# Kernel optimization log

Measured on AMD Instinct MI355X. Metric: run time of the kernel, lower is better.

The kernel has to match this reference:

```python
import jax, jax.numpy as jnp
import numpy as np

N, C, K, KEIG, B, NG, H = 32768, 128, 5, 128, 64, 512, 4
E = 524288
EPS = 1e-5


def setup_inputs() -> dict:
    key = jax.random.key(0)
    ks = iter(jax.random.split(key, 40))
    def nrm(shape, scale):
        return jax.random.normal(next(ks), shape, jnp.float32) * scale
    s = 1.0 / np.sqrt(C)
    return dict(
        x=nrm((N, C), 1.0),
        U=nrm((N, KEIG), 1.0 / np.sqrt(N)),
        Lambda=jax.random.uniform(next(ks), (KEIG,), jnp.float32, 0.0, 2.0),
        lambda_max=jnp.full((1,), 2.0, jnp.float32),
        w_spa1=nrm((C, C), s), b_spa1=jnp.zeros((C,), jnp.float32),
        w_spa2=nrm((C, C), s), b_spa2=jnp.zeros((C,), jnp.float32),
        w_spe1=nrm((C, C), s), b_spe1=jnp.zeros((C,), jnp.float32),
        w_spe2=nrm((C, C), s), b_spe2=jnp.zeros((C,), jnp.float32),
        cheb_w=nrm((K, C, C), s), cheb_b=jnp.zeros((C,), jnp.float32),
        gamma=jnp.ones((1,), jnp.float32),
        w_proj=nrm((C, C), s),
        w_qkv=nrm((C, 3 * C), s), b_qkv=jnp.zeros((3 * C,), jnp.float32),
        w_out=nrm((C, C), s), b_out=jnp.zeros((C,), jnp.float32),
        mlp_w1=nrm((C, 2 * C), s), mlp_b1=jnp.zeros((2 * C,), jnp.float32),
        mlp_w2=nrm((2 * C, C), 1.0 / np.sqrt(2 * C)), mlp_b2=jnp.zeros((C,), jnp.float32),
        bn1_w=jnp.ones((C,), jnp.float32), bn1_b=jnp.zeros((C,), jnp.float32),
        bn2_w=jnp.ones((C,), jnp.float32), bn2_b=jnp.zeros((C,), jnp.float32),
        bn3_w=jnp.ones((C,), jnp.float32), bn3_b=jnp.zeros((C,), jnp.float32),
        edge_index=jax.random.randint(next(ks), (2, E), 0, N, jnp.int64) if jax.config.jax_enable_x64 else jax.random.randint(next(ks), (2, E), 0, N, jnp.int32),
        batch=jnp.repeat(jnp.arange(B), NG),  # 64 graphs of 512 nodes each
    )


def _mlp2(h, w1, b1, w2, b2):
    return jnp.maximum(h @ w1 + b1, 0.0) @ w2 + b2


def _bn(h, w, b):
    # train-mode BatchNorm1d over node dim (biased variance), GPSConv default norm
    mu = h.mean(0)
    var = jnp.mean((h - mu) ** 2, 0)
    return (h - mu) * jax.lax.rsqrt(var + EPS) * w + b


def _cheb(x, src, dst, lam, Ws, bias):
    # L_hat = (2/lambda_max) * (I - D^{-1/2} A D^{-1/2}) - I ; sym normalization
    deg = jax.ops.segment_sum(jnp.ones_like(src, x.dtype), src, num_segments=N)
    dis = jnp.where(deg > 0, 1.0 / jnp.sqrt(deg), 0.0)
    w = dis[src] * dis[dst]  # [E]
    scale = 2.0 / lam
    def lhat(v):
        agg = jax.ops.segment_sum(w[:, None] * v[src], dst, num_segments=N)
        return (scale - 1.0) * v - scale * agg
    Tx0 = x
    out = Tx0 @ Ws[0]
    Tx1 = lhat(Tx0)
    out = out + Tx1 @ Ws[1]
    for k in range(2, K):
        Tx2 = 2.0 * lhat(Tx1) - Tx0
        out = out + Tx2 @ Ws[k]
        Tx0, Tx1 = Tx1, Tx2
    return out + bias


def _mha(xd, w_qkv, b_qkv, w_out, b_out):
    Bq, n, _ = xd.shape
    dh = C // H
    qkv = xd @ w_qkv + b_qkv  # [B,n,3C]
    q, k, v = jnp.split(qkv, 3, axis=-1)
    heads = lambda t: t.reshape(Bq, n, H, dh).transpose(0, 2, 1, 3)
    q, k, v = heads(q), heads(k), heads(v)
    a = jax.nn.softmax(jnp.einsum('bhqd,bhkd->bhqk', q, k) / np.sqrt(dh), axis=-1)
    o = jnp.einsum('bhqk,bhkd->bhqd', a, v).transpose(0, 2, 1, 3).reshape(Bq, n, C)
    return o @ w_out + b_out


def reference(x, U, Lambda, lambda_max,
              w_spa1, b_spa1, w_spa2, b_spa2,
              w_spe1, b_spe1, w_spe2, b_spe2,
              cheb_w, cheb_b, gamma, w_proj,
              w_qkv, b_qkv, w_out, b_out,
              mlp_w1, mlp_b1, mlp_w2, mlp_b2,
              bn1_w, bn1_b, bn2_w, bn2_b, bn3_w, bn3_b,
              edge_index, batch):
    src, dst = edge_index[0], edge_index[1]
    lam = lambda_max[0]
    # ---- SpectralLocalNN (GPSConv local conv branch) ----
    x_sp = _mlp2(x, w_spa1, b_spa1, w_spa2, b_spa2)
    out_local = _cheb(x_sp, src, dst, lam, cheb_w, cheb_b)
    x_spec = _mlp2(x, w_spe1, b_spe1, w_spe2, b_spe2)
    h_proj = x_spec @ w_proj
    s_lam = jnp.exp(-gamma[0] * Lambda ** 2)  # [k_eig]
    out_spectral = U @ (s_lam[:, None] * (U.T @ h_proj))
    h1 = _bn(out_local + out_spectral + x, bn1_w, bn1_b)
    # ---- global attention branch (equal-size graphs -> dense reshape) ----
    xd = x.reshape(B, NG, C)
    h2 = _mha(xd, w_qkv, b_qkv, w_out, b_out).reshape(N, C)
    h2 = _bn(h2 + x, bn2_w, bn2_b)
    # ---- combine + MLP ----
    out = h1 + h2
    out = out + _mlp2(out, mlp_w1, mlp_b1, mlp_w2, mlp_b2)
    return _bn(out, bn3_w, bn3_b)
```

## Files before the change

### kernel.cpp

```cpp
#include <hip/hip_runtime.h>

typedef short bf16x8 __attribute__((ext_vector_type(8)));
typedef short bf16x4 __attribute__((ext_vector_type(4)));
typedef float f32x4 __attribute__((ext_vector_type(4)));

#define DEVI __device__ __forceinline__

constexpr int N   = 32768;
constexpr int C   = 128;
constexpr int E   = 524288;
constexpr float EPSV = 1e-5f;
constexpr int UT_BLOCKS = 256;
constexpr int HB  = 64;
constexpr int EPB = E / HB;
constexpr float QSCALE = 0.17677669529663687f * 1.4426950408889634f;

DEVI float bf2f(ushort u){ return __uint_as_float(((uint)u) << 16); }
DEVI ushort f2bf(float f){
  uint u = __float_as_uint(f);
  return (ushort)((u + 0x7fffu + ((u >> 16) & 1u)) >> 16);
}
DEVI uint cvtpk(float lo, float hi){
  uint r;
  asm("v_cvt_pk_bf16_f32 %0, %1, %2" : "=v"(r) : "v"(lo), "v"(hi));
  return r;
}
DEVI float fexp2(float x){
  float r;
  asm("v_exp_f32 %0, %1" : "=v"(r) : "v"(x));
  return r;
}
DEVI float sane(float v){ if (!(v == v)) return 0.f; return fminf(fmaxf(v, -1e30f), 1e30f); }
DEVI bool mode_fp32(const uint* lmraw){ return (lmraw[0] & 0xffffu) == 0u; }

constexpr int CSZ[28] = {128,1,16384,128,16384,128,16384,128,16384,128,81920,128,
                         1,16384,49152,384,16384,128,32768,256,32768,128,
                         128,128,128,128,128,128};
constexpr int COF[28] = {0,128,192,16576,16704,33088,33216,49600,49728,66112,
                         66240,148160,148288,148352,164736,213888,214272,230656,
                         230784,263552,263808,296576,296704,296832,296960,297088,
                         297216,297344};
constexpr int CAN_SMALL_TOTAL = 297472;

struct CvtArgs { const void* src[28]; };

__global__ __launch_bounds__(256) void convert_small(CvtArgs a, ushort* __restrict__ can,
                                                     const uint* __restrict__ lmraw)
{
  bool f32 = mode_fp32(lmraw);
  int idx = blockIdx.x * 256 + threadIdx.x;
  #pragma unroll 1
  for (int s = 0; s < 28; s++) {
    if (idx < CSZ[s]) {
      ushort v = f32 ? f2bf(((const float*)a.src[s])[idx])
                     : ((const ushort*)a.src[s])[idx];
      can[COF[s] + idx] = v;
      return;
    }
    idx -= CSZ[s];
  }
}

__global__ __launch_bounds__(256) void convert_big(const void* __restrict__ xs,
    const void* __restrict__ Us, ushort* __restrict__ canx, ushort* __restrict__ canu,
    const uint* __restrict__ lmraw)
{
  bool f32 = mode_fp32(lmraw);
  size_t e = ((size_t)blockIdx.x * 256 + threadIdx.x) * 4;
  bool isU = e >= (size_t)N * C;
  size_t off = isU ? e - (size_t)N * C : e;
  const void* src = isU ? Us : xs;
  ushort* dst = isU ? canu : canx;
  ushort4 o;
  if (f32) {
    float4 v = *(const float4*)((const float*)src + off);
    o.x = f2bf(v.x); o.y = f2bf(v.y); o.z = f2bf(v.z); o.w = f2bf(v.w);
  } else {
    o = *(const ushort4*)((const ushort*)src + off);
  }
  *(ushort4*)(dst + off) = o;
}

__global__ __launch_bounds__(1024) void hist_lds(const int* __restrict__ ei,
    int* __restrict__ cei, ushort* __restrict__ part)
{
  __shared__ uint hist[N / 2];
  int t = threadIdx.x;
  int b = blockIdx.x;
  bool i64 = ((ei[1] | ei[3] | ei[5] | ei[7]) == 0);
  size_t j0 = (size_t)b * EPB;
  #pragma unroll
  for (int i = t; i < N / 2; i += 1024) hist[i] = 0u;
  __syncthreads();
  for (int k = t; k < EPB; k += 1024) {
    size_t j = j0 + k;
    int v = (i64 ? ei[2 * j] : ei[j]) & (N - 1);
    cei[j] = v;
    atomicAdd(&hist[v >> 1], 1u << ((v & 1) * 16));
  }
  __syncthreads();
  uint* po = (uint*)(part + (size_t)b * N);
  for (int i = t; i < N / 2; i += 1024) po[i] = hist[i];
}

__global__ __launch_bounds__(256) void reduce_cnt(const ushort* __restrict__ part,
    int* __restrict__ cdt, float* __restrict__ dis)
{
  int d = blockIdx.x * 256 + threadIdx.x;
  int s = 0, tt = 0;
  #pragma unroll 8
  for (int b = 0; b < HB; b++) s  += part[(size_t)b * N + d];
  #pragma unroll 8
  for (int b = 0; b < HB; b++) tt += part[(size_t)(HB + b) * N + d];
  cdt[d] = tt;
  dis[d] = s > 0 ? rsqrtf((float)s) : 0.f;
}

__global__ __launch_bounds__(1024) void scan_kernel(const int* __restrict__ cnt,
                                                    int* __restrict__ row_ptr)
{
  __shared__ int sums[1024];
  int t = threadIdx.x;
  int loc[32]; int s = 0;
  int base = t * 32;
  #pragma unroll
  for (int i = 0; i < 32; i++) { loc[i] = s; s += cnt[base + i]; }
  sums[t] = s;
  __syncthreads();
  for (int off = 1; off < 1024; off <<= 1) {
    int v = (t >= off) ? sums[t - off] : 0;
    __syncthreads();
    sums[t] += v;
    __syncthreads();
  }
  int pre = (t == 0) ? 0 : sums[t - 1];
  #pragma unroll
  for (int i = 0; i < 32; i++) row_ptr[base + i] = pre + loc[i];
}

__global__ __launch_bounds__(256) void off_kernel(const int* __restrict__ rp,
    const ushort* __restrict__ part, int* __restrict__ off2)
{
  int d = blockIdx.x * 256 + threadIdx.x;
  int run = rp[d];
  #pragma unroll 8
  for (int b = 0; b < HB; b++) {
    off2[(size_t)b * N + d] = run;
    run += part[(size_t)(HB + b) * N + d];
  }
}

__global__ __launch_bounds__(1024) void edge_scatter(const int* __restrict__ cei,
    const int* __restrict__ off2, const float* __restrict__ dis,
    int2* __restrict__ ep)
{
  __shared__ int base[N];
  int t = threadIdx.x;
  int b = blockIdx.x;
  for (int i = t; i < N; i += 1024) base[i] = off2[(size_t)b * N + i];
  __syncthreads();
  size_t e0 = (size_t)b * EPB;
  for (int k = t; k < EPB; k += 1024) {
    size_t e = e0 + k;
    int s = cei[e], d = cei[e + E];
    int slot = atomicAdd(&base[d], 1);
    int2 v; v.x = s; v.y = __float_as_int(dis[s] * dis[d]);
    ep[slot] = v;
  }
}

constexpr int WT_SPA1 = 0;
constexpr int WT_SPA2 = 16384;
constexpr int WT_SPE1 = 32768;
constexpr int WT_SPE2 = 49152;
constexpr int WT_PROJ = 65536;
constexpr int WT_CHEB = 81920;
constexpr int WT_QKV  = 163840;
constexpr int WT_WOUT = 212992;
constexpr int WT_MLP1 = 229376;
constexpr int WT_MLP2 = 262144;
constexpr int WT_TOTAL = 294912;

__global__ __launch_bounds__(256) void zero_kernel(int* __restrict__ p, int n)
{
  int i = blockIdx.x * 256 + threadIdx.x;
  if (i < n) p[i] = 0;
}

__global__ __launch_bounds__(256) void transpose_weights(
    const ushort* __restrict__ spa1, const ushort* __restrict__ spa2,
    const ushort* __restrict__ spe1, const ushort* __restrict__ spe2,
    const ushort* __restrict__ proj, const ushort* __restrict__ cheb,
    const ushort* __restrict__ qkv,  const ushort* __restrict__ wout,
    const ushort* __restrict__ mlp1, const ushort* __restrict__ mlp2,
    ushort* __restrict__ wt)
{
  int i = blockIdx.x * 256 + threadIdx.x;
  if (i < 81920) {
    int m = i >> 14, r = i & 16383; int k = r >> 7, n = r & 127;
    const ushort* src = m==0?spa1 : m==1?spa2 : m==2?spe1 : m==3?spe2 : proj;
    wt[m*16384 + n*128 + k] = src[r];
  } else if (i < 163840) {
    int j = i - 81920; int m = j >> 14, r = j & 16383; int k = r >> 7, n = r & 127;
    wt[WT_CHEB + n*640 + m*128 + k] = cheb[j];
  } else if (i < 212992) {
    int j = i - 163840; int k = j / 384, n = j % 384;
    wt[WT_QKV + n*128 + k] = qkv[j];
  } else if (i < 229376) {
    int j = i - 212992; int k = j >> 7, n = j & 127;
    wt[WT_WOUT + n*128 + k] = wout[j];
  } else if (i < 262144) {
    int j = i - 229376; int k = j >> 8, n = j & 255;
    wt[WT_MLP1 + n*128 + k] = mlp1[j];
  } else if (i < WT_TOTAL) {
    int j = i - 262144; int k = j >> 7, n = j & 127;
    wt[WT_MLP2 + n*256 + k] = mlp2[j];
  }
}

template<int K, int COLS, bool RELU, int OMODE, bool BIAS, bool RES, int ASTR, int OSTR, bool QSC>
__global__ __launch_bounds__(256) void gemm_lds(
    const ushort* __restrict__ A, const ushort* __restrict__ WT,
    const ushort* __restrict__ bias, const ushort* __restrict__ res,
    void* __restrict__ outp)
{
  constexpr int NSEG = COLS / 128;
  constexpr int NKC = K / 128;
  constexpr int BP = 136;
  __shared__ ushort Bs[128 * BP];
  int tid = threadIdx.x;
  int lane = tid & 63, wave = tid >> 6;
  int quad = lane >> 4, l16 = lane & 15;
  int seg = (NSEG > 1) ? (blockIdx.x % NSEG) : 0;
  int rb  = (NSEG > 1) ? (blockIdx.x / NSEG) : blockIdx.x;
  int row0 = rb * 64 + wave * 16;
  const ushort* wseg = WT + (size_t)(seg * 128) * K;

  f32x4 acc[8];
  #pragma unroll
  for (int nt = 0; nt < 8; nt++) acc[nt] = (f32x4){0.f, 0.f, 0.f, 0.f};

  for (int kc = 0; kc < NKC; kc++) {
    if (kc) __syncthreads();
    #pragma unroll
    for (int i = tid; i < 2048; i += 256) {
      int col = i >> 4, ko = (i & 15) * 8;
      *(bf16x8*)&Bs[col * BP + ko] =
          *(const bf16x8*)(wseg + (size_t)col * K + kc * 128 + ko);
    }
    __syncthreads();
    bf16x8 a[4];
    const ushort* ap = A + (size_t)(row0 + l16) * ASTR + kc * 128 + quad * 8;
    #pragma unroll
    for (int kk = 0; kk < 4; kk++) a[kk] = *(const bf16x8*)(ap + kk * 32);
    #pragma unroll
    for (int kk = 0; kk < 4; kk++) {
      #pragma unroll
      for (int nt = 0; nt < 8; nt++) {
        bf16x8 b = *(const bf16x8*)(&Bs[(nt * 16 + l16) * BP + kk * 32 + quad * 8]);
        acc[nt] = __builtin_amdgcn_mfma_f32_16x16x32_bf16(a[kk], b, acc[nt], 0, 0, 0);
      }
    }
  }

  #pragma unroll
  for (int nt = 0; nt < 8; nt++) {
    int col = seg * 128 + nt * 16 + l16;
    float bv = 0.f;
    if (BIAS) bv = bf2f(bias[col]);
    #pragma unroll
    for (int r = 0; r < 4; r++) {
      int row = row0 + quad * 4 + r;
      size_t oi = (size_t)row * OSTR + col;
      float v = acc[nt][r] + bv;
      if (RES) v += bf2f(res[(size_t)row * COLS + col]);
      if (RELU) v = fmaxf(v, 0.f);
      if (QSC && col < 128) v *= QSCALE;
      if (OMODE == 0)      ((ushort*)outp)[oi] = f2bf(v);
      else if (OMODE == 1) ((float*)outp)[oi] = v;
      else                 ((float*)outp)[oi] += v;
    }
  }
}

__global__ __launch_bounds__(256) void spmm_cheb(
    const int* __restrict__ row_ptr, const int2* __restrict__ ep,
    const ushort* __restrict__ v,
    const ushort* __restrict__ txprev, ushort* __restrict__ txout,
    const ushort* __restrict__ lambda_max, int first, int str)
{
  int wave = threadIdx.x >> 6, lane = threadIdx.x & 63;
  int sub = lane >> 4, l16 = lane & 15;
  int d = blockIdx.x * 4 + wave;
  float lm = bf2f(lambda_max[0]);
  float scale = 2.f / lm;
  if (!(scale == scale) || fabsf(scale) > 1e6f) scale = 1.f;
  int beg = row_ptr[d];
  int end = (d == N - 1) ? E : row_ptr[d + 1];
  float acc[8] = {0.f,0.f,0.f,0.f,0.f,0.f,0.f,0.f};
  for (int jb = beg; jb < end; jb += 4) {
    int j = jb + sub;
    bool ok = j < end;
    int2 e2 = ep[ok ? j : beg];
    int s = e2.x & (N - 1);
    float w = ok ? __int_as_float(e2.y) : 0.f;
    bf16x8 vv = *(const bf16x8*)(v + (size_t)s * str + l16 * 8);
    #pragma unroll
    for (int i = 0; i < 8; i++) acc[i] += w * bf2f((ushort)vv[i]);
  }
  #pragma unroll
  for (int i = 0; i < 8; i++) {
    acc[i] += __shfl_xor(acc[i], 16);
    acc[i] += __shfl_xor(acc[i], 32);
  }
  if (sub == 0) {
    bf16x8 vd = *(const bf16x8*)(v + (size_t)d * str + l16 * 8);
    bf16x8 tp;
    if (!first) tp = *(const bf16x8*)(txprev + (size_t)d * str + l16 * 8);
    bf16x8 ov;
    #pragma unroll
    for (int i = 0; i < 8; i++) {
      float r = (scale - 1.f) * bf2f((ushort)vd[i]) - scale * acc[i];
      if (!first) r = 2.f * r - bf2f((ushort)tp[i]);
      ov[i] = (short)f2bf(r);
    }
    *(bf16x8*)(txout + (size_t)d * str + l16 * 8) = ov;
  }
}

__global__ __launch_bounds__(256) void ut_mfma(const ushort* __restrict__ U,
    const ushort* __restrict__ hp, float* __restrict__ parts)
{
  constexpr int RP = 40;
  __shared__ ushort Ut[128 * RP];
  __shared__ ushort Ht[128 * RP];
  int t = threadIdx.x;
  int lane = t & 63, wave = t >> 6;
  int quad = lane >> 4, l16 = lane & 15;

  f32x4 acc[2][8];
  #pragma unroll
  for (int a = 0; a < 2; a++)
    #pragma unroll
    for (int ct = 0; ct < 8; ct++) acc[a][ct] = (f32x4){0.f, 0.f, 0.f, 0.f};

  for (int ch = 0; ch < 4; ch++) {
    int n0 = blockIdx.x * 128 + ch * 32;
    __syncthreads();
    for (int i = t; i < 2048; i += 256) {
      int r2 = i >> 7, c = i & 127;
      uint u0 = U [(size_t)(n0 + r2 * 2) * 128 + c];
      uint u1 = U [(size_t)(n0 + r2 * 2 + 1) * 128 + c];
      *(uint*)&Ut[c * RP + r2 * 2] = (u0 & 0xffffu) | (u1 << 16);
      uint h0 = hp[(size_t)(n0 + r2 * 2) * 128 + c];
      uint h1 = hp[(size_t)(n0 + r2 * 2 + 1) * 128 + c];
      *(uint*)&Ht[c * RP + r2 * 2] = (h0 & 0xffffu) | (h1 << 16);
    }
    __syncthreads();
    bf16x8 bfr[8];
    #pragma unroll
    for (int ct = 0; ct < 8; ct++)
      bfr[ct] = *(const bf16x8*)(&Ht[(ct * 16 + l16) * RP + quad * 8]);
    #pragma unroll
    for (int a = 0; a < 2; a++) {
      int kt = wave * 2 + a;
      bf16x8 af = *(const bf16x8*)(&Ut[(kt * 16 + l16) * RP + quad * 8]);
      #pragma unroll
      for (int ct = 0; ct < 8; ct++)
        acc[a][ct] = __builtin_amdgcn_mfma_f32_16x16x32_bf16(af, bfr[ct], acc[a][ct], 0, 0, 0);
    }
  }

  float* po = parts + (size_t)blockIdx.x * 16384;
  #pragma unroll
  for (int a = 0; a < 2; a++) {
    int kt = wave * 2 + a;
    #pragma unroll
    for (int ct = 0; ct < 8; ct++)
      #pragma unroll
      for (int r = 0; r < 4; r++)
        po[(kt * 16 + quad * 4 + r) * 128 + ct * 16 + l16] = acc[a][ct][r];
  }
}

__global__ __launch_bounds__(256) void reduce_mt(const float* __restrict__ parts,
    const ushort* __restrict__ Lambda, const ushort* __restrict__ gamma,
    ushort* __restrict__ MT)
{
  int e = blockIdx.x * 256 + threadIdx.x;
  int keig = e >> 7, c = e & 127;
  float s = 0.f;
  for (int p = 0; p < UT_BLOCKS; p++) s += parts[(size_t)p * 16384 + e];
  float g = bf2f(gamma[0]);
  float lam = bf2f(Lambda[keig]);
  float sl = __expf(-g * lam * lam);
  MT[c * 128 + keig] = f2bf(sl * s);
}

__global__ __launch_bounds__(256) void bn_stats(const float* __restrict__ h,
                                                float* __restrict__ stats)
{
  int c = threadIdx.x & 127, half = threadIdx.x >> 7;
  int r0 = blockIdx.x * 128 + half;
  float s = 0.f, s2 = 0.f;
  for (int i = 0; i < 64; i++) {
    float v = sane(h[(size_t)(r0 + i * 2) * 128 + c]);
    s += v; s2 += v * v;
  }
  atomicAdd(&stats[c], s);
  atomicAdd(&stats[128 + c], s2);
}

__global__ __launch_bounds__(256) void bn_apply(const float* __restrict__ h,
    const float* __restrict__ st, const ushort* __restrict__ gw,
    const ushort* __restrict__ gb, const ushort* __restrict__ add,
    void* __restrict__ out, const uint* __restrict__ lmraw, int final_out)
{
  size_t e = ((size_t)blockIdx.x * 256 + threadIdx.x) * 4;
  int c0 = (int)(e & 127);
  float4 hv = *(const float4*)(h + e);
  float xv[4] = {sane(hv.x), sane(hv.y), sane(hv.z), sane(hv.w)};
  float addv[4] = {0.f, 0.f, 0.f, 0.f};
  if (add) {
    ushort4 av = *(const ushort4*)(add + e);
    addv[0] = bf2f(av.x); addv[1] = bf2f(av.y);
    addv[2] = bf2f(av.z); addv[3] = bf2f(av.w);
  }
  float r[4];
  #pragma unroll
  for (int j = 0; j < 4; j++) {
    int c = c0 + j;
    float mu = st[c] * (1.f / 32768.f);
    float var = fmaxf(st[128 + c] * (1.f / 32768.f) - mu * mu, 0.f);
    r[j] = (xv[j] - mu) * rsqrtf(var + EPSV) * bf2f(gw[c]) + bf2f(gb[c]) + addv[j];
  }
  if (final_out && mode_fp32(lmraw)) {
    float4 o4; o4.x = r[0]; o4.y = r[1]; o4.z = r[2]; o4.w = r[3];
    *(float4*)((float*)out + e) = o4;
  } else {
    ushort4 o;
    o.x = f2bf(r[0]); o.y = f2bf(r[1]); o.z = f2bf(r[2]); o.w = f2bf(r[3]);
    *(ushort4*)((ushort*)out + e) = o;
  }
}

__global__ __launch_bounds__(512) void attn_mfma(const ushort* __restrict__ qkv,
                                                 ushort* __restrict__ attn)
{
  constexpr int VP = 516;
  constexpr int KP = 40;
  __shared__ ushort Kt[512 * KP];
  __shared__ ushort Vt[32 * VP];
  int b = blockIdx.x;
  int g = b >> 3, hh = (b >> 1) & 3, half = b & 1;
  int lane = threadIdx.x & 63, wave = threadIdx.x >> 6;
  int quad = lane >> 4, l16 = lane & 15;
  const ushort* base = qkv + (size_t)g * 512 * 384;

  for (int i = threadIdx.x; i < 512 * 4; i += 512) {
    int key = i >> 2, c8 = (i & 3) * 8;
    *(bf16x8*)&Kt[key * KP + c8] =
        *(const bf16x8*)(base + (size_t)key * 384 + 128 + hh * 32 + c8);
  }
  for (int i = threadIdx.x; i < 256 * 8; i += 512) {
    int kp = i >> 3, d4 = (i & 7) * 4;
    const ushort* va = base + (size_t)(2 * kp) * 384 + 256 + hh * 32 + d4;
    ushort4 a = *(const ushort4*)va;
    ushort4 c = *(const ushort4*)(va + 384);
    *(uint*)&Vt[(d4 + 0) * VP + 2 * kp] = (uint)a.x | ((uint)c.x << 16);
    *(uint*)&Vt[(d4 + 1) * VP + 2 * kp] = (uint)a.y | ((uint)c.y << 16);
    *(uint*)&Vt[(d4 + 2) * VP + 2 * kp] = (uint)a.z | ((uint)c.z << 16);
    *(uint*)&Vt[(d4 + 3) * VP + 2 * kp] = (uint)a.w | ((uint)c.w << 16);
  }
  __syncthreads();

  int q0 = half * 256 + wave * 32;
  bf16x8 qf[2];
  #pragma unroll
  for (int i = 0; i < 2; i++)
    qf[i] = *(const bf16x8*)(base + (size_t)(q0 + i * 16 + l16) * 384 + hh * 32 + quad * 8);

  f32x4 O[2][2];
  #pragma unroll
  for (int dt = 0; dt < 2; dt++)
    #pragma unroll
    for (int i = 0; i < 2; i++) O[dt][i] = (f32x4){0.f, 0.f, 0.f, 0.f};
  float lsum[2] = {0.f, 0.f};

  union PU { uint u[4]; bf16x8 v; };
  union VU { uint2 a[2]; bf16x8 v; };

  for (int kt2 = 0; kt2 < 16; kt2++) {
    int k0 = kt2 * 32;
    bf16x8 kfA = *(const bf16x8*)&Kt[(k0 + l16) * KP + quad * 8];
    bf16x8 kfB = *(const bf16x8*)&Kt[(k0 + 16 + l16) * KP + quad * 8];
    PU pw[2];
    #pragma unroll
    for (int i = 0; i < 2; i++) {
      f32x4 sA = __builtin_amdgcn_mfma_f32_16x16x32_bf16(kfA, qf[i], (f32x4){0.f,0.f,0.f,0.f}, 0, 0, 0);
      f32x4 sB = __builtin_amdgcn_mfma_f32_16x16x32_bf16(kfB, qf[i], (f32x4){0.f,0.f,0.f,0.f}, 0, 0, 0);
      float p0 = fexp2(fminf(sA[0], 86.5f));
      float p1 = fexp2(fminf(sA[1], 86.5f));
      float p2 = fexp2(fminf(sA[2], 86.5f));
      float p3 = fexp2(fminf(sA[3], 86.5f));
      float p4 = fexp2(fminf(sB[0], 86.5f));
      float p5 = fexp2(fminf(sB[1], 86.5f));
      float p6 = fexp2(fminf(sB[2], 86.5f));
      float p7 = fexp2(fminf(sB[3], 86.5f));
      lsum[i] += ((p0 + p1) + (p2 + p3)) + ((p4 + p5) + (p6 + p7));
      pw[i].u[0] = cvtpk(p0, p1); pw[i].u[1] = cvtpk(p2, p3);
      pw[i].u[2] = cvtpk(p4, p5); pw[i].u[3] = cvtpk(p6, p7);
    }
    #pragma unroll
    for (int dt = 0; dt < 2; dt++) {
      int drow = (dt * 16 + l16) * VP;
      VU vu;
      vu.a[0] = *(const uint2*)&Vt[drow + k0 + quad * 4];
      vu.a[1] = *(const uint2*)&Vt[drow + k0 + 16 + quad * 4];
      #pragma unroll
      for (int i = 0; i < 2; i++)
        O[dt][i] = __builtin_amdgcn_mfma_f32_16x16x32_bf16(vu.v, pw[i].v, O[dt][i], 0, 0, 0);
    }
  }

  #pragma unroll
  for (int i = 0; i < 2; i++) {
    float l = lsum[i];
    l += __shfl_xor(l, 16);
    l += __shfl_xor(l, 32);
    lsum[i] = 1.f / l;
  }

  #pragma unroll
  for (int i = 0; i < 2; i++) {
    size_t node = (size_t)g * 512 + q0 + i * 16 + l16;
    #pragma unroll
    for (int dt = 0; dt < 2; dt++) {
      uint2 o;
      o.x = cvtpk(O[dt][i][0] * lsum[i], O[dt][i][1] * lsum[i]);
      o.y = cvtpk(O[dt][i][2] * lsum[i], O[dt][i][3] * lsum[i]);
      *(uint2*)(attn + node * 128 + hh * 32 + dt * 16 + quad * 4) = o;
    }
  }
}

constexpr size_t KB = 1024;
constexpr size_t MB = 1048576;
constexpr size_t OFF_WT    = 0;
constexpr size_t OFF_CDT   = 576 * KB;
constexpr size_t OFF_RP    = 704 * KB;
constexpr size_t OFF_DIS   = 832 * KB;
constexpr size_t OFF_MT    = 960 * KB;
constexpr size_t OFF_STATS = 1024 * KB;
constexpr size_t OFF_CEI   = 6  * MB;
constexpr size_t OFF_EP    = 10 * MB;
constexpr size_t OFF_CANX  = 14 * MB;
constexpr size_t OFF_CANU  = 22 * MB;
constexpr size_t OFF_CANS  = 30 * MB;
constexpr size_t OFF_F1    = 31 * MB;
constexpr size_t OFF_SPEC  = 31 * MB;
constexpr size_t OFF_HPROJ = 39 * MB;
constexpr size_t OFF_TBIG  = 47 * MB;
constexpr size_t OFF_PARTH = OFF_TBIG;
constexpr size_t OFF_OFF2  = OFF_TBIG + 8 * MB;
constexpr size_t OFF_PARTS = 87 * MB;

extern "C" void kernel_launch(void* const* d_in, const int* in_sizes, int n_in,
                              void* d_out, int out_size, void* d_ws, size_t ws_size,
                              hipStream_t stream) {
  (void)in_sizes; (void)n_in; (void)out_size; (void)ws_size;
  const uint* lmraw = (const uint*)d_in[3];
  const int*  ei    = (const int*)d_in[30];

  char* W = (char*)d_ws;
  ushort* wt    = (ushort*)(W + OFF_WT);
  int*    cdt   = (int*)(W + OFF_CDT);
  int*    rp    = (int*)(W + OFF_RP);
  float*  dis   = (float*)(W + OFF_DIS);
  ushort* MT    = (ushort*)(W + OFF_MT);
  float*  stats = (float*)(W + OFF_STATS);
  int*    cei   = (int*)(W + OFF_CEI);
  int2*   ep    = (int2*)(W + OFF_EP);
  ushort* part  = (ushort*)(W + OFF_PARTH);
  int*    off2  = (int*)(W + OFF_OFF2);
  ushort* canx  = (ushort*)(W + OFF_CANX);
  ushort* canu  = (ushort*)(W + OFF_CANU);
  ushort* cs    = (ushort*)(W + OFF_CANS);
  float*  F1    = (float*)(W + OFF_F1);
  ushort* spec  = (ushort*)(W + OFF_SPEC);
  ushort* tmpA  = (ushort*)(W + OFF_HPROJ);
  ushort* hproj = (ushort*)(W + OFF_HPROJ);
  ushort* Tbig  = (ushort*)(W + OFF_TBIG);
  ushort* qkvb  = (ushort*)(W + OFF_TBIG);
  ushort* mlph  = (ushort*)(W + OFF_TBIG);
  float*  parts = (float*)(W + OFF_PARTS);
  ushort* attnb = (ushort*)(W + OFF_PARTS);
  ushort* h1    = (ushort*)(W + OFF_CANU);
  ushort* comb  = (ushort*)(W + OFF_CANX);

  const ushort* cLambda = cs + COF[0];
  const ushort* cLmx    = cs + COF[1];
  const ushort* cSpa1   = cs + COF[2];
  const ushort* cBspa1  = cs + COF[3];
  const ushort* cSpa2   = cs + COF[4];
  const ushort* cBspa2  = cs + COF[5];
  const ushort* cSpe1   = cs + COF[6];
  const ushort* cBspe1  = cs + COF[7];
  const ushort* cSpe2   = cs + COF[8];
  const ushort* cBspe2  = cs + COF[9];
  const ushort* cCheb   = cs + COF[10];
  const ushort* cChebB  = cs + COF[11];
  const ushort* cGam    = cs + COF[12];
  const ushort* cProj   = cs + COF[13];
  const ushort* cQkv    = cs + COF[14];
  const ushort* cBqkv   = cs + COF[15];
  const ushort* cWout   = cs + COF[16];
  const ushort* cBout   = cs + COF[17];
  const ushort* cMw1    = cs + COF[18];
  const ushort* cMb1    = cs + COF[19];
  const ushort* cMw2    = cs + COF[20];
  const ushort* cMb2    = cs + COF[21];
  const ushort* cBn1w   = cs + COF[22];
  const ushort* cBn1b   = cs + COF[23];
  const ushort* cBn2w   = cs + COF[24];
  const ushort* cBn2b   = cs + COF[25];
  const ushort* cBn3w   = cs + COF[26];
  const ushort* cBn3b   = cs + COF[27];

  const ushort* NUL = nullptr;

  zero_kernel<<<3, 256, 0, stream>>>((int*)(W + OFF_STATS), 768);

  CvtArgs ca;
  ca.src[0]  = d_in[2];  ca.src[1]  = d_in[3];  ca.src[2]  = d_in[4];
  ca.src[3]  = d_in[5];  ca.src[4]  = d_in[6];  ca.src[5]  = d_in[7];
  ca.src[6]  = d_in[8];  ca.src[7]  = d_in[9];  ca.src[8]  = d_in[10];
  ca.src[9]  = d_in[11]; ca.src[10] = d_in[12]; ca.src[11] = d_in[13];
  ca.src[12] = d_in[14]; ca.src[13] = d_in[15]; ca.src[14] = d_in[16];
  ca.src[15] = d_in[17]; ca.src[16] = d_in[18]; ca.src[17] = d_in[19];
  ca.src[18] = d_in[20]; ca.src[19] = d_in[21]; ca.src[20] = d_in[22];
  ca.src[21] = d_in[23]; ca.src[22] = d_in[24]; ca.src[23] = d_in[25];
  ca.src[24] = d_in[26]; ca.src[25] = d_in[27]; ca.src[26] = d_in[28];
  ca.src[27] = d_in[29];
  convert_small<<<(CAN_SMALL_TOTAL + 255) / 256, 256, 0, stream>>>(ca, cs, lmraw);
  convert_big<<<(2 * N * C / 4) / 256, 256, 0, stream>>>(d_in[0], d_in[1], canx, canu, lmraw);

  transpose_weights<<<1152, 256, 0, stream>>>(cSpa1, cSpa2, cSpe1, cSpe2,
      cProj, cCheb, cQkv, cWout, cMw1, cMw2, wt);

  hist_lds<<<2 * HB, 1024, 0, stream>>>(ei, cei, part);
  reduce_cnt<<<N / 256, 256, 0, stream>>>(part, cdt, dis);
  scan_kernel<<<1, 1024, 0, stream>>>(cdt, rp);
  off_kernel<<<N / 256, 256, 0, stream>>>(rp, part, off2);
  edge_scatter<<<HB, 1024, 0, stream>>>(cei, off2, dis, ep);

  dim3 g1(512), g2(1024), g3(1536), bb(256);
  gemm_lds<128,128,true ,0,true ,false,128,128,false><<<g1, bb, 0, stream>>>(canx, wt + WT_SPA1, cBspa1, NUL, tmpA);
  gemm_lds<128,128,false,0,true ,false,128,640,false><<<g1, bb, 0, stream>>>(tmpA, wt + WT_SPA2, cBspa2, NUL, Tbig);
  gemm_lds<128,128,true ,0,true ,false,128,128,false><<<g1, bb, 0, stream>>>(canx, wt + WT_SPE1, cBspe1, NUL, tmpA);
  gemm_lds<128,128,false,0,true ,false,128,128,false><<<g1, bb, 0, stream>>>(tmpA, wt + WT_SPE2, cBspe2, NUL, spec);
  gemm_lds<128,128,false,0,false,false,128,128,false><<<g1, bb, 0, stream>>>(spec, wt + WT_PROJ, NUL,    NUL, hproj);

  ut_mfma<<<UT_BLOCKS, 256, 0, stream>>>(canu, hproj, parts);
  reduce_mt<<<64, 256, 0, stream>>>(parts, cLambda, cGam, MT);

  spmm_cheb<<<N / 4, 256, 0, stream>>>(rp, ep, Tbig,       NUL,        Tbig + 128, cLmx, 1, 640);
  spmm_cheb<<<N / 4, 256, 0, stream>>>(rp, ep, Tbig + 128, Tbig,       Tbig + 256, cLmx, 0, 640);
  spmm_cheb<<<N / 4, 256, 0, stream>>>(rp, ep, Tbig + 256, Tbig + 128, Tbig + 384, cLmx, 0, 640);
  spmm_cheb<<<N / 4, 256, 0, stream>>>(rp, ep, Tbig + 384, Tbig + 256, Tbig + 512, cLmx, 0, 640);
  gemm_lds<640,128,false,1,true ,false,640,128,false><<<g1, bb, 0, stream>>>(Tbig, wt + WT_CHEB, cChebB, NUL, F1);

  gemm_lds<128,128,false,2,false,true ,128,128,false><<<g1, bb, 0, stream>>>(canu, MT, NUL, canx, F1);
  bn_stats<<<256, 256, 0, stream>>>(F1, stats);
  bn_apply<<<(N * C) / 1024, 256, 0, stream>>>(F1, stats, cBn1w, cBn1b, NUL, h1, lmraw, 0);

  gemm_lds<128,384,false,0,true ,false,128,384,true ><<<g3, bb, 0, stream>>>(canx, wt + WT_QKV, cBqkv, NUL, qkvb);
  attn_mfma<<<512, 512, 0, stream>>>(qkvb, attnb);
  gemm_lds<128,128,false,1,true ,true ,128,128,false><<<g1, bb, 0, stream>>>(attnb, wt + WT_WOUT, cBout, canx, F1);
  bn_stats<<<256, 256, 0, stream>>>(F1, stats + 256);
  bn_apply<<<(N * C) / 1024, 256, 0, stream>>>(F1, stats + 256, cBn2w, cBn2b, h1, comb, lmraw, 0);

  gemm_lds<128,256,true ,0,true ,false,128,256,false><<<g2, bb, 0, stream>>>(comb, wt + WT_MLP1, cMb1, NUL, mlph);
  gemm_lds<256,128,false,1,true ,true ,256,128,false><<<g1, bb, 0, stream>>>(mlph, wt + WT_MLP2, cMb2, comb, F1);
  bn_stats<<<256, 256, 0, stream>>>(F1, stats + 512);
  bn_apply<<<(N * C) / 1024, 256, 0, stream>>>(F1, stats + 512, cBn3w, cBn3b, NUL, d_out, lmraw, 1);
}
```

Before: 540.9 us.

## Fuse chained 128x128 GEMMs and MLP into single LDS-resident kernels

```diff
diff --git a/kernel.cpp b/kernel.cpp
--- a/kernel.cpp
+++ b/kernel.cpp
@@ -10,7 +10,7 @@
 constexpr int C   = 128;
 constexpr int E   = 524288;
 constexpr float EPSV = 1e-5f;
-constexpr int UT_BLOCKS = 256;
+constexpr int UT_BLOCKS = 128;
 constexpr int HB  = 64;
 constexpr int EPB = E / HB;
 constexpr float QSCALE = 0.17677669529663687f * 1.4426950408889634f;
@@ -283,6 +283,209 @@
   }
 }
 
+template<bool THIRD, int OSTR>
+__global__ __launch_bounds__(256) void gemm_chain(
+    const ushort* __restrict__ A,
+    const ushort* __restrict__ W1, const ushort* __restrict__ B1,
+    const ushort* __restrict__ W2, const ushort* __restrict__ B2,
+    const ushort* __restrict__ W3,
+    ushort* __restrict__ outp)
+{
+  constexpr int BP = 136;
+  __shared__ ushort Bs[128 * BP];
+  __shared__ ushort Ts[64 * BP];
+  int tid = threadIdx.x;
+  int lane = tid & 63, wave = tid >> 6;
+  int quad = lane >> 4, l16 = lane & 15;
+  int row0 = blockIdx.x * 64 + wave * 16;
+  int lw = wave * 16;
+
+  for (int i = tid; i < 2048; i += 256) {
+    int col = i >> 4, ko = (i & 15) * 8;
+    *(bf16x8*)&Bs[col * BP + ko] = *(const bf16x8*)(W1 + (size_t)col * 128 + ko);
+  }
+  __syncthreads();
+  bf16x8 a[4];
+  {
+    const ushort* ap = A + (size_t)(row0 + l16) * 128 + quad * 8;
+    #pragma unroll
+    for (int kk = 0; kk < 4; kk++) a[kk] = *(const bf16x8*)(ap + kk * 32);
+  }
+  f32x4 acc[8];
+  #pragma unroll
+  for (int nt = 0; nt < 8; nt++) acc[nt] = (f32x4){0.f, 0.f, 0.f, 0.f};
+  #pragma unroll
+  for (int kk = 0; kk < 4; kk++)
+    #pragma unroll
+    for (int nt = 0; nt < 8; nt++) {
+      bf16x8 b = *(const bf16x8*)(&Bs[(nt * 16 + l16) * BP + kk * 32 + quad * 8]);
+      acc[nt] = __builtin_amdgcn_mfma_f32_16x16x32_bf16(a[kk], b, acc[nt], 0, 0, 0);
+    }
+  #pragma unroll
+  for (int nt = 0; nt < 8; nt++) {
+    int col = nt * 16 + l16;
+    float bv = bf2f(B1[col]);
+    #pragma unroll
+    for (int r = 0; r < 4; r++)
+      Ts[(lw + quad * 4 + r) * BP + col] = f2bf(fmaxf(acc[nt][r] + bv, 0.f));
+  }
+  __syncthreads();
+
+  for (int i = tid; i < 2048; i += 256) {
+    int col = i >> 4, ko = (i & 15) * 8;
+    *(bf16x8*)&Bs[col * BP + ko] = *(const bf16x8*)(W2 + (size_t)col * 128 + ko);
+  }
+  #pragma unroll
+  for (int kk = 0; kk < 4; kk++)
+    a[kk] = *(const bf16x8*)(&Ts[(lw + l16) * BP + kk * 32 + quad * 8]);
+  __syncthreads();
+  #pragma unroll
+  for (int nt = 0; nt < 8; nt++) acc[nt] = (f32x4){0.f, 0.f, 0.f, 0.f};
+  #pragma unroll
+  for (int kk = 0; kk < 4; kk++)
+    #pragma unroll
+    for (int nt = 0; nt < 8; nt++) {
+      bf16x8 b = *(const bf16x8*)(&Bs[(nt * 16 + l16) * BP + kk * 32 + quad * 8]);
+      acc[nt] = __builtin_amdgcn_mfma_f32_16x16x32_bf16(a[kk], b, acc[nt], 0, 0, 0);
+    }
+
+  if (!THIRD) {
+    #pragma unroll
+    for (int nt = 0; nt < 8; nt++) {
+      int col = nt * 16 + l16;
+      float bv = bf2f(B2[col]);
+      #pragma unroll
+      for (int r = 0; r < 4; r++)
+        outp[(size_t)(row0 + quad * 4 + r) * OSTR + col] = f2bf(acc[nt][r] + bv);
+    }
+    return;
+  }
+
+  __syncthreads();
+  #pragma unroll
+  for (int nt = 0; nt < 8; nt++) {
+    int col = nt * 16 + l16;
+    float bv = bf2f(B2[col]);
+    #pragma unroll
+    for (int r = 0; r < 4; r++)
+      Ts[(lw + quad * 4 + r) * BP + col] = f2bf(acc[nt][r] + bv);
+  }
+  __syncthreads();
+  for (int i = tid; i < 2048; i += 256) {
+    int col = i >> 4, ko = (i & 15) * 8;
+    *(bf16x8*)&Bs[col * BP + ko] = *(const bf16x8*)(W3 + (size_t)col * 128 + ko);
+  }
+  #pragma unroll
+  for (int kk = 0; kk < 4; kk++)
+    a[kk] = *(const bf16x8*)(&Ts[(lw + l16) * BP + kk * 32 + quad * 8]);
+  __syncthreads();
+  #pragma unroll
+  for (int nt = 0; nt < 8; nt++) acc[nt] = (f32x4){0.f, 0.f, 0.f, 0.f};
+  #pragma unroll
+  for (int kk = 0; kk < 4; kk++)
+    #pragma unroll
+    for (int nt = 0; nt < 8; nt++) {
+      bf16x8 b = *(const bf16x8*)(&Bs[(nt * 16 + l16) * BP + kk * 32 + quad * 8]);
+      acc[nt] = __builtin_amdgcn_mfma_f32_16x16x32_bf16(a[kk], b, acc[nt], 0, 0, 0);
+    }
+  #pragma unroll
+  for (int nt = 0; nt < 8; nt++) {
+    int col = nt * 16 + l16;
+    #pragma unroll
+    for (int r = 0; r < 4; r++)
+      outp[(size_t)(row0 + quad * 4 + r) * OSTR + col] = f2bf(acc[nt][r]);
+  }
+}
+
+__global__ __launch_bounds__(256) void gemm_mlp(
+    const ushort* __restrict__ A,
+    const ushort* __restrict__ W1, const ushort* __restrict__ B1,
+    const ushort* __restrict__ W2, const ushort* __restrict__ B2,
+    const ushort* __restrict__ res, float* __restrict__ outp)
+{
+  constexpr int BP = 136;
+  constexpr int HP = 264;
+  __shared__ ushort Bs[128 * BP];
+  __shared__ ushort Hs[64 * HP];
+  int tid = threadIdx.x;
+  int lane = tid & 63, wave = tid >> 6;
+  int quad = lane >> 4, l16 = lane & 15;
+  int row0 = blockIdx.x * 64 + wave * 16;
+  int lw = wave * 16;
+
+  bf16x8 a[4];
+  {
+    const ushort* ap = A + (size_t)(row0 + l16) * 128 + quad * 8;
+    #pragma unroll
+    for (int kk = 0; kk < 4; kk++) a[kk] = *(const bf16x8*)(ap + kk * 32);
+  }
+
+  for (int seg = 0; seg < 2; seg++) {
+    if (seg) __syncthreads();
+    for (int i = tid; i < 2048; i += 256) {
+      int col = i >> 4, ko = (i & 15) * 8;
+      *(bf16x8*)&Bs[col * BP + ko] =
+          *(const bf16x8*)(W1 + (size_t)(seg * 128 + col) * 128 + ko);
+    }
+    __syncthreads();
+    f32x4 acc[8];
+    #pragma unroll
+    for (int nt = 0; nt < 8; nt++) acc[nt] = (f32x4){0.f, 0.f, 0.f, 0.f};
+    #pragma unroll
+    for (int kk = 0; kk < 4; kk++)
+      #pragma unroll
+      for (int nt = 0; nt < 8; nt++) {
+        bf16x8 b = *(const bf16x8*)(&Bs[(nt * 16 + l16) * BP + kk * 32 + quad * 8]);
+        acc[nt] = __builtin_amdgcn_mfma_f32_16x16x32_bf16(a[kk], b, acc[nt], 0, 0, 0);
+      }
+    #pragma unroll
+    for (int nt = 0; nt < 8; nt++) {
+      int col = seg * 128 + nt * 16 + l16;
+      float bv = bf2f(B1[col]);
+      #pragma unroll
+      for (int r = 0; r < 4; r++)
+        Hs[(lw + quad * 4 + r) * HP + col] = f2bf(fmaxf(acc[nt][r] + bv, 0.f));
+    }
+  }
+  __syncthreads();
+
+  f32x4 acc2[8];
+  #pragma unroll
+  for (int nt = 0; nt < 8; nt++) acc2[nt] = (f32x4){0.f, 0.f, 0.f, 0.f};
+  for (int kc = 0; kc < 2; kc++) {
+    if (kc) __syncthreads();
+    for (int i = tid; i < 2048; i += 256) {
+      int col = i >> 4, ko = (i & 15) * 8;
+      *(bf16x8*)&Bs[col * BP + ko] =
+          *(const bf16x8*)(W2 + (size_t)col * 256 + kc * 128 + ko);
+    }
+    bf16x8 a2[4];
+    #pragma unroll
+    for (int kk = 0; kk < 4; kk++)
+      a2[kk] = *(const bf16x8*)(&Hs[(lw + l16) * HP + kc * 128 + kk * 32 + quad * 8]);
+    __syncthreads();
+    #pragma unroll
+    for (int kk = 0; kk < 4; kk++)
+      #pragma unroll
+      for (int nt = 0; nt < 8; nt++) {
+        bf16x8 b = *(const bf16x8*)(&Bs[(nt * 16 + l16) * BP + kk * 32 + quad * 8]);
+        acc2[nt] = __builtin_amdgcn_mfma_f32_16x16x32_bf16(a2[kk], b, acc2[nt], 0, 0, 0);
+      }
+  }
+
+  #pragma unroll
+  for (int nt = 0; nt < 8; nt++) {
+    int col = nt * 16 + l16;
+    float bv = bf2f(B2[col]);
+    #pragma unroll
+    for (int r = 0; r < 4; r++) {
+      int row = row0 + quad * 4 + r;
+      float v = acc2[nt][r] + bv + bf2f(res[(size_t)row * 128 + col]);
+      outp[(size_t)row * 128 + col] = v;
+    }
+  }
+}
+
 __global__ __launch_bounds__(256) void spmm_cheb(
     const int* __restrict__ row_ptr, const int2* __restrict__ ep,
     const ushort* __restrict__ v,
@@ -344,8 +547,8 @@
     #pragma unroll
     for (int ct = 0; ct < 8; ct++) acc[a][ct] = (f32x4){0.f, 0.f, 0.f, 0.f};
 
-  for (int ch = 0; ch < 4; ch++) {
-    int n0 = blockIdx.x * 128 + ch * 32;
+  for (int ch = 0; ch < 8; ch++) {
+    int n0 = blockIdx.x * 256 + ch * 32;
     __syncthreads();
     for (int i = t; i < 2048; i += 256) {
       int r2 = i >> 7, c = i & 127;
@@ -558,7 +761,6 @@
 constexpr size_t OFF_CANU  = 22 * MB;
 constexpr size_t OFF_CANS  = 30 * MB;
 constexpr size_t OFF_F1    = 31 * MB;
-constexpr size_t OFF_SPEC  = 31 * MB;
 constexpr size_t OFF_HPROJ = 39 * MB;
 constexpr size_t OFF_TBIG  = 47 * MB;
 constexpr size_t OFF_PARTH = OFF_TBIG;
@@ -587,12 +789,9 @@
   ushort* canu  = (ushort*)(W + OFF_CANU);
   ushort* cs    = (ushort*)(W + OFF_CANS);
   float*  F1    = (float*)(W + OFF_F1);
-  ushort* spec  = (ushort*)(W + OFF_SPEC);
-  ushort* tmpA  = (ushort*)(W + OFF_HPROJ);
   ushort* hproj = (ushort*)(W + OFF_HPROJ);
   ushort* Tbig  = (ushort*)(W + OFF_TBIG);
   ushort* qkvb  = (ushort*)(W + OFF_TBIG);
-  ushort* mlph  = (ushort*)(W + OFF_TBIG);
   float*  parts = (float*)(W + OFF_PARTS);
   ushort* attnb = (ushort*)(W + OFF_PARTS);
   ushort* h1    = (ushort*)(W + OFF_CANU);
@@ -600,25 +799,15 @@
 
   const ushort* cLambda = cs + COF[0];
   const ushort* cLmx    = cs + COF[1];
-  const ushort* cSpa1   = cs + COF[2];
   const ushort* cBspa1  = cs + COF[3];
-  const ushort* cSpa2   = cs + COF[4];
   const ushort* cBspa2  = cs + COF[5];
-  const ushort* cSpe1   = cs + COF[6];
   const ushort* cBspe1  = cs + COF[7];
-  const ushort* cSpe2   = cs + COF[8];
   const ushort* cBspe2  = cs + COF[9];
-  const ushort* cCheb   = cs + COF[10];
   const ushort* cChebB  = cs + COF[11];
   const ushort* cGam    = cs + COF[12];
-  const ushort* cProj   = cs + COF[13];
-  const ushort* cQkv    = cs + COF[14];
   const ushort* cBqkv   = cs + COF[15];
-  const ushort* cWout   = cs + COF[16];
   const ushort* cBout   = cs + COF[17];
-  const ushort* cMw1    = cs + COF[18];
   const ushort* cMb1    = cs + COF[19];
-  const ushort* cMw2    = cs + COF[20];
   const ushort* cMb2    = cs + COF[21];
   const ushort* cBn1w   = cs + COF[22];
   const ushort* cBn1b   = cs + COF[23];
@@ -645,8 +834,9 @@
   convert_small<<<(CAN_SMALL_TOTAL + 255) / 256, 256, 0, stream>>>(ca, cs, lmraw);
   convert_big<<<(2 * N * C / 4) / 256, 256, 0, stream>>>(d_in[0], d_in[1], canx, canu, lmraw);
 
-  transpose_weights<<<1152, 256, 0, stream>>>(cSpa1, cSpa2, cSpe1, cSpe2,
-      cProj, cCheb, cQkv, cWout, cMw1, cMw2, wt);
+  transpose_weights<<<1152, 256, 0, stream>>>(cs + COF[2], cs + COF[4], cs + COF[6],
+      cs + COF[8], cs + COF[13], cs + COF[10], cs + COF[14], cs + COF[16],
+      cs + COF[18], cs + COF[20], wt);
 
   hist_lds<<<2 * HB, 1024, 0, stream>>>(ei, cei, part);
   reduce_cnt<<<N / 256, 256, 0, stream>>>(part, cdt, dis);
@@ -654,12 +844,11 @@
   off_kernel<<<N / 256, 256, 0, stream>>>(rp, part, off2);
   edge_scatter<<<HB, 1024, 0, stream>>>(cei, off2, dis, ep);
 
-  dim3 g1(512), g2(1024), g3(1536), bb(256);
-  gemm_lds<128,128,true ,0,true ,false,128,128,false><<<g1, bb, 0, stream>>>(canx, wt + WT_SPA1, cBspa1, NUL, tmpA);
-  gemm_lds<128,128,false,0,true ,false,128,640,false><<<g1, bb, 0, stream>>>(tmpA, wt + WT_SPA2, cBspa2, NUL, Tbig);
-  gemm_lds<128,128,true ,0,true ,false,128,128,false><<<g1, bb, 0, stream>>>(canx, wt + WT_SPE1, cBspe1, NUL, tmpA);
-  gemm_lds<128,128,false,0,true ,false,128,128,false><<<g1, bb, 0, stream>>>(tmpA, wt + WT_SPE2, cBspe2, NUL, spec);
-  gemm_lds<128,128,false,0,false,false,128,128,false><<<g1, bb, 0, stream>>>(spec, wt + WT_PROJ, NUL,    NUL, hproj);
+  dim3 g1(512), g3(1536), bb(256);
+  gemm_chain<false, 640><<<g1, bb, 0, stream>>>(canx, wt + WT_SPA1, cBspa1,
+      wt + WT_SPA2, cBspa2, NUL, Tbig);
+  gemm_chain<true, 128><<<g1, bb, 0, stream>>>(canx, wt + WT_SPE1, cBspe1,
+      wt + WT_SPE2, cBspe2, wt + WT_PROJ, hproj);
 
   ut_mfma<<<UT_BLOCKS, 256, 0, stream>>>(canu, hproj, parts);
   reduce_mt<<<64, 256, 0, stream>>>(parts, cLambda, cGam, MT);
@@ -680,8 +869,7 @@
   bn_stats<<<256, 256, 0, stream>>>(F1, stats + 256);
   bn_apply<<<(N * C) / 1024, 256, 0, stream>>>(F1, stats + 256, cBn2w, cBn2b, h1, comb, lmraw, 0);
 
-  gemm_lds<128,256,true ,0,true ,false,128,256,false><<<g2, bb, 0, stream>>>(comb, wt + WT_MLP1, cMb1, NUL, mlph);
-  gemm_lds<256,128,false,1,true ,true ,256,128,false><<<g1, bb, 0, stream>>>(mlph, wt + WT_MLP2, cMb2, comb, F1);
+  gemm_mlp<<<g1, bb, 0, stream>>>(comb, wt + WT_MLP1, cMb1, wt + WT_MLP2, cMb2, comb, F1);
   bn_stats<<<256, 256, 0, stream>>>(F1, stats + 512);
   bn_apply<<<(N * C) / 1024, 256, 0, stream>>>(F1, stats + 512, cBn3w, cBn3b, NUL, d_out, lmraw, 1);
 }
```

Result: no change. 538.3 us (-0.5%).
